# Performance work log

Measured on AMD Instinct MI355X. Metric: run time of the kernel, lower is better.

## Reference

```python
import jax, jax.numpy as jnp
import numpy as np

N_EMBD = 1024
N_HEAD = 16
HEAD_DIM = N_EMBD // N_HEAD
SCALE = HEAD_DIM ** -0.5


def setup_inputs() -> dict:
    key = jax.random.key(0)
    ks = jax.random.split(key, 6)
    B, T = 64, 256
    s = N_EMBD ** -0.5
    return {
        "x": jax.random.normal(ks[0], (B, T, N_EMBD), dtype=jnp.float32),
        "Wq": jax.random.normal(ks[1], (N_EMBD, N_EMBD), dtype=jnp.float32) * s,
        "Wk": jax.random.normal(ks[2], (N_EMBD, N_EMBD), dtype=jnp.float32) * s,
        "Wv": jax.random.normal(ks[3], (N_EMBD, N_EMBD), dtype=jnp.float32) * s,
        "Wo": jax.random.normal(ks[4], (N_EMBD, N_EMBD), dtype=jnp.float32) * s,
        "bo": jax.random.normal(ks[5], (N_EMBD,), dtype=jnp.float32) * 0.01,
    }


def reference(x, Wq, Wk, Wv, Wo, bo):
    B, T, C = x.shape
    # QKV projections (no bias), split heads -> [B, H, T, Dh]
    def heads(y):
        return y.reshape(B, T, N_HEAD, HEAD_DIM).transpose(0, 2, 1, 3)
    q = heads(x @ Wq)
    k = heads(x @ Wk)
    v = heads(x @ Wv)
    # scaled causal attention scores [B, H, T, T]
    wei = jnp.einsum("bhqd,bhkd->bhqk", q, k) * SCALE
    causal = jnp.tril(jnp.ones((T, T), dtype=bool))
    wei = jnp.where(causal, wei, -jnp.inf)
    wei = jax.nn.softmax(wei, axis=-1)
    # dropout is identity in eval mode
    out = jnp.einsum("bhqk,bhkd->bhqd", wei, v)
    out = out.transpose(0, 2, 1, 3).reshape(B, T, C)
    return out @ Wo + bo
```

## Files before the change

### kernel.cpp

```cpp
#include <hip/hip_runtime.h>
#include <hip/hip_bf16.h>
#include <stdint.h>

typedef __attribute__((ext_vector_type(8))) short bfx8;
typedef __attribute__((ext_vector_type(4))) short bfx4;
typedef __attribute__((ext_vector_type(4))) float f32x4;
typedef __attribute__((ext_vector_type(4))) unsigned short us4;

#define SCALE_ATT 0.125f

__device__ __forceinline__ unsigned short f2bf(float f) {
  union { float f; unsigned u; } a; a.f = f;
  unsigned r = a.u + 0x7fffu + ((a.u >> 16) & 1u);
  return (unsigned short)(r >> 16);
}

__device__ __forceinline__ void gll16(const void* g, void* l) {
  __builtin_amdgcn_global_load_lds(
      (__attribute__((address_space(1))) void*)(g),
      (__attribute__((address_space(3))) void*)(l), 16, 0, 0);
}

__device__ __forceinline__ bfx8 ld2x64(const unsigned short* p) {
  bfx4 lo = *(const bfx4*)p;
  bfx4 hi = *(const bfx4*)(p + 4);
  return __builtin_shufflevector(lo, hi, 0, 1, 2, 3, 4, 5, 6, 7);
}

__global__ __launch_bounds__(256) void cvt_x(const float* __restrict__ x,
                                             unsigned short* __restrict__ xb, int n4) {
  int i = blockIdx.x * blockDim.x + threadIdx.x;
  int stride = gridDim.x * blockDim.x;
  const float4* x4 = (const float4*)x;
  for (; i < n4; i += stride) {
    float4 v = x4[i];
    us4 o;
    o[0] = f2bf(v.x); o[1] = f2bf(v.y); o[2] = f2bf(v.z); o[3] = f2bf(v.w);
    *(us4*)&xb[(size_t)i * 4] = o;
  }
}

__global__ __launch_bounds__(256) void cvt_w(const float* __restrict__ W0, const float* __restrict__ W1,
                                             const float* __restrict__ W2, const float* __restrict__ W3,
                                             unsigned short* __restrict__ T0, unsigned short* __restrict__ T1,
                                             unsigned short* __restrict__ T2, unsigned short* __restrict__ T3) {
  const float* W; unsigned short* T;
  switch (blockIdx.z) {
    case 0: W = W0; T = T0; break;
    case 1: W = W1; T = T1; break;
    case 2: W = W2; T = T2; break;
    default: W = W3; T = T3; break;
  }
  __shared__ unsigned short Ts[64][68];
  int k0 = blockIdx.x * 64, n0 = blockIdx.y * 64;
  int t = threadIdx.x;
  int lrow = t >> 4, c4 = t & 15;
  #pragma unroll
  for (int i = 0; i < 4; i++) {
    int row = lrow + i * 16;
    float4 v = *(const float4*)&W[(size_t)(k0 + row) * 1024 + n0 + c4 * 4];
    Ts[c4 * 4 + 0][row] = f2bf(v.x);
    Ts[c4 * 4 + 1][row] = f2bf(v.y);
    Ts[c4 * 4 + 2][row] = f2bf(v.z);
    Ts[c4 * 4 + 3][row] = f2bf(v.w);
  }
  __syncthreads();
  #pragma unroll
  for (int i = 0; i < 4; i++) {
    int nrow = lrow + i * 16;
    us4 v = *(const us4*)&Ts[nrow][c4 * 4];
    *(us4*)&T[(size_t)(n0 + nrow) * 1024 + k0 + c4 * 4] = v;
  }
}

__global__ __launch_bounds__(256) void gemm_qkv(
    const unsigned short* __restrict__ A,
    const unsigned short* __restrict__ Wtq, const unsigned short* __restrict__ Wtk,
    const unsigned short* __restrict__ Wtv,
    unsigned short* __restrict__ Qb, unsigned short* __restrict__ Kb, unsigned short* __restrict__ Vb) {
  __shared__ unsigned short As[128 * 32];
  __shared__ unsigned short Bs[128 * 32];
  int t = threadIdx.x;
  int w = t >> 6, l = t & 63;
  int wr = w >> 1, wc = w & 1;
  int lr = l & 15, lh = l >> 4;
  int bm = blockIdx.x, bn = blockIdx.y;
  int sel = bn >> 3;
  int n0 = (bn & 7) * 128;
  const unsigned short* Bt = sel == 0 ? Wtq : (sel == 1 ? Wtk : Wtv);
  unsigned short* Out = sel == 0 ? Qb : (sel == 1 ? Kb : Vb);

  const unsigned short* Ag = A + (size_t)(bm * 128) * 1024;
  const unsigned short* Bg = Bt + (size_t)n0 * 1024;

  f32x4 acc[4][4];
  #pragma unroll
  for (int i = 0; i < 4; i++)
    #pragma unroll
    for (int j = 0; j < 4; j++) acc[i][j] = (f32x4){0.f, 0.f, 0.f, 0.f};

  int srow = w * 32 + (l >> 2);
  int sk = (l & 3) * 8;

  for (int k0 = 0; k0 < 1024; k0 += 32) {
    gll16(Ag + (size_t)srow * 1024 + k0 + sk,        As + w * 1024);
    gll16(Ag + (size_t)(srow + 16) * 1024 + k0 + sk, As + w * 1024 + 512);
    gll16(Bg + (size_t)srow * 1024 + k0 + sk,        Bs + w * 1024);
    gll16(Bg + (size_t)(srow + 16) * 1024 + k0 + sk, Bs + w * 1024 + 512);
    __syncthreads();
    bfx8 af[4], bfv[4];
    #pragma unroll
    for (int rt = 0; rt < 4; rt++) af[rt] = *(const bfx8*)&As[(wr * 64 + rt * 16 + lr) * 32 + lh * 8];
    #pragma unroll
    for (int ct = 0; ct < 4; ct++) bfv[ct] = *(const bfx8*)&Bs[(wc * 64 + ct * 16 + lr) * 32 + lh * 8];
    #pragma unroll
    for (int rt = 0; rt < 4; rt++)
      #pragma unroll
      for (int ct = 0; ct < 4; ct++)
        acc[rt][ct] = __builtin_amdgcn_mfma_f32_16x16x32_bf16(af[rt], bfv[ct], acc[rt][ct], 0, 0, 0);
    __syncthreads();
  }

  int row0 = bm * 128 + wr * 64;
  #pragma unroll
  for (int rt = 0; rt < 4; rt++)
    #pragma unroll
    for (int ct = 0; ct < 4; ct++)
      #pragma unroll
      for (int j = 0; j < 4; j++) {
        int r = row0 + rt * 16 + lh * 4 + j;
        int c = n0 + wc * 64 + ct * 16 + lr;
        Out[(size_t)r * 1024 + c] = f2bf(acc[rt][ct][j]);
      }
}

__global__ __launch_bounds__(256) void gemm_proj(
    const unsigned short* __restrict__ A, const unsigned short* __restrict__ Bt,
    const float* __restrict__ bias, float* __restrict__ Out) {
  __shared__ unsigned short As[128 * 32];
  __shared__ unsigned short Bs[128 * 32];
  int t = threadIdx.x;
  int w = t >> 6, l = t & 63;
  int wr = w >> 1, wc = w & 1;
  int lr = l & 15, lh = l >> 4;
  int bm = blockIdx.x, bn = blockIdx.y;
  int n0 = bn * 128;
  const unsigned short* Ag = A + (size_t)(bm * 128) * 1024;
  const unsigned short* Bg = Bt + (size_t)n0 * 1024;

  f32x4 acc[4][4];
  #pragma unroll
  for (int i = 0; i < 4; i++)
    #pragma unroll
    for (int j = 0; j < 4; j++) acc[i][j] = (f32x4){0.f, 0.f, 0.f, 0.f};

  int srow = w * 32 + (l >> 2);
  int sk = (l & 3) * 8;

  for (int k0 = 0; k0 < 1024; k0 += 32) {
    gll16(Ag + (size_t)srow * 1024 + k0 + sk,        As + w * 1024);
    gll16(Ag + (size_t)(srow + 16) * 1024 + k0 + sk, As + w * 1024 + 512);
    gll16(Bg + (size_t)srow * 1024 + k0 + sk,        Bs + w * 1024);
    gll16(Bg + (size_t)(srow + 16) * 1024 + k0 + sk, Bs + w * 1024 + 512);
    __syncthreads();
    bfx8 af[4], bfv[4];
    #pragma unroll
    for (int rt = 0; rt < 4; rt++) af[rt] = *(const bfx8*)&As[(wr * 64 + rt * 16 + lr) * 32 + lh * 8];
    #pragma unroll
    for (int ct = 0; ct < 4; ct++) bfv[ct] = *(const bfx8*)&Bs[(wc * 64 + ct * 16 + lr) * 32 + lh * 8];
    #pragma unroll
    for (int rt = 0; rt < 4; rt++)
      #pragma unroll
      for (int ct = 0; ct < 4; ct++)
        acc[rt][ct] = __builtin_amdgcn_mfma_f32_16x16x32_bf16(af[rt], bfv[ct], acc[rt][ct], 0, 0, 0);
    __syncthreads();
  }

  float bv[4];
  #pragma unroll
  for (int ct = 0; ct < 4; ct++) bv[ct] = bias[n0 + wc * 64 + ct * 16 + lr];

  int row0 = bm * 128 + wr * 64;
  #pragma unroll
  for (int rt = 0; rt < 4; rt++)
    #pragma unroll
    for (int ct = 0; ct < 4; ct++)
      #pragma unroll
      for (int j = 0; j < 4; j++) {
        int r = row0 + rt * 16 + lh * 4 + j;
        int c = n0 + wc * 64 + ct * 16 + lr;
        Out[(size_t)r * 1024 + c] = acc[rt][ct][j] + bv[ct];
      }
}

__global__ __launch_bounds__(256) void attn_kernel(
    const unsigned short* __restrict__ Qb, const unsigned short* __restrict__ Kb,
    const unsigned short* __restrict__ Vb, unsigned short* __restrict__ Ab) {
  __shared__ unsigned short Vt[64][260];
  __shared__ unsigned short Pw[4][16][36];

  int t = threadIdx.x;
  int w = t >> 6, l = t & 63;
  int lr = l & 15, lh = l >> 4;
  int bh = blockIdx.x;
  size_t rowbase = (size_t)(bh >> 4) * 256 * 1024 + (size_t)(bh & 15) * 64;

  {
    int rr = t >> 3, part = t & 7;
    for (int i = 0; i < 8; i++) {
      int row = i * 32 + rr;
      bfx8 vv = *(const bfx8*)(Vb + rowbase + (size_t)row * 1024 + part * 8);
      #pragma unroll
      for (int e = 0; e < 8; e++) Vt[part * 8 + e][row] = (unsigned short)vv[e];
    }
  }
  __syncthreads();

  for (int qt = 0; qt < 4; qt++) {
    int r0 = qt * 64 + w * 16;
    const unsigned short* Qrow = Qb + rowbase + (size_t)(r0 + lr) * 1024 + lh * 8;
    bfx8 aq0 = *(const bfx8*)(Qrow);
    bfx8 aq1 = *(const bfx8*)(Qrow + 32);

    float m[4], lsum[4];
    #pragma unroll
    for (int j = 0; j < 4; j++) { m[j] = -1e30f; lsum[j] = 0.f; }
    f32x4 oc[4];
    #pragma unroll
    for (int ct = 0; ct < 4; ct++) oc[ct] = (f32x4){0.f, 0.f, 0.f, 0.f};

    int nkc = ((r0 + 15) >> 5) + 1;
    for (int kc = 0; kc < nkc; kc++) {
      const unsigned short* Kr = Kb + rowbase + (size_t)(kc * 32 + lr) * 1024 + lh * 8;
      bfx8 bk00 = *(const bfx8*)(Kr);
      bfx8 bk01 = *(const bfx8*)(Kr + 32);
      bfx8 bk10 = *(const bfx8*)(Kr + 16 * 1024);
      bfx8 bk11 = *(const bfx8*)(Kr + 16 * 1024 + 32);
      f32x4 s0 = (f32x4){0.f, 0.f, 0.f, 0.f};
      f32x4 s1 = (f32x4){0.f, 0.f, 0.f, 0.f};
      s0 = __builtin_amdgcn_mfma_f32_16x16x32_bf16(aq0, bk00, s0, 0, 0, 0);
      s0 = __builtin_amdgcn_mfma_f32_16x16x32_bf16(aq1, bk01, s0, 0, 0, 0);
      s1 = __builtin_amdgcn_mfma_f32_16x16x32_bf16(aq0, bk10, s1, 0, 0, 0);
      s1 = __builtin_amdgcn_mfma_f32_16x16x32_bf16(aq1, bk11, s1, 0, 0, 0);

      int c0 = kc * 32 + lr, c1 = c0 + 16;
      #pragma unroll
      for (int j = 0; j < 4; j++) {
        int row = r0 + lh * 4 + j;
        float v0 = (c0 <= row) ? s0[j] : -1e30f;
        float v1 = (c1 <= row) ? s1[j] : -1e30f;
        float cm = fmaxf(v0, v1);
        cm = fmaxf(cm, __shfl_xor(cm, 1));
        cm = fmaxf(cm, __shfl_xor(cm, 2));
        cm = fmaxf(cm, __shfl_xor(cm, 4));
        cm = fmaxf(cm, __shfl_xor(cm, 8));
        float mn = fmaxf(m[j], cm);
        float sc = __expf((m[j] - mn) * SCALE_ATT);
        float p0 = (c0 <= row) ? __expf((s0[j] - mn) * SCALE_ATT) : 0.f;
        float p1 = (c1 <= row) ? __expf((s1[j] - mn) * SCALE_ATT) : 0.f;
        m[j] = mn;
        float cs = p0 + p1;
        cs += __shfl_xor(cs, 1);
        cs += __shfl_xor(cs, 2);
        cs += __shfl_xor(cs, 4);
        cs += __shfl_xor(cs, 8);
        lsum[j] = lsum[j] * sc + cs;
        #pragma unroll
        for (int ct = 0; ct < 4; ct++) oc[ct][j] *= sc;
        Pw[w][lh * 4 + j][lr] = f2bf(p0);
        Pw[w][lh * 4 + j][16 + lr] = f2bf(p1);
      }

      bfx8 pa = ld2x64(&Pw[w][lr][lh * 8]);
      #pragma unroll
      for (int ct = 0; ct < 4; ct++) {
        bfx8 vb = ld2x64(&Vt[ct * 16 + lr][kc * 32 + lh * 8]);
        oc[ct] = __builtin_amdgcn_mfma_f32_16x16x32_bf16(pa, vb, oc[ct], 0, 0, 0);
      }
    }

    float rinv[4];
    #pragma unroll
    for (int j = 0; j < 4; j++) rinv[j] = 1.0f / lsum[j];
    #pragma unroll
    for (int ct = 0; ct < 4; ct++)
      #pragma unroll
      for (int j = 0; j < 4; j++) {
        int row = r0 + lh * 4 + j;
        Ab[rowbase + (size_t)row * 1024 + ct * 16 + lr] = f2bf(oc[ct][j] * rinv[j]);
      }
  }
}

extern "C" void kernel_launch(void* const* d_in, const int* in_sizes, int n_in,
                              void* d_out, int out_size, void* d_ws, size_t ws_size,
                              hipStream_t stream) {
  const float* x  = (const float*)d_in[0];
  const float* Wq = (const float*)d_in[1];
  const float* Wk = (const float*)d_in[2];
  const float* Wv = (const float*)d_in[3];
  const float* Wo = (const float*)d_in[4];
  const float* bo = (const float*)d_in[5];
  float* out = (float*)d_out;

  char* ws = (char*)d_ws;
  unsigned short* xb  = (unsigned short*)(ws);
  unsigned short* Wtq = (unsigned short*)(ws + (size_t)(32u << 20));
  unsigned short* Wtk = (unsigned short*)(ws + (size_t)(34u << 20));
  unsigned short* Wtv = (unsigned short*)(ws + (size_t)(36u << 20));
  unsigned short* Wto = (unsigned short*)(ws + (size_t)(38u << 20));
  unsigned short* Qb  = (unsigned short*)(ws + (size_t)(40u << 20));
  unsigned short* Kb  = (unsigned short*)(ws + (size_t)(72u << 20));
  unsigned short* Vb  = (unsigned short*)(ws + (size_t)(104u << 20));
  unsigned short* Ab  = xb;

  cvt_x<<<2048, 256, 0, stream>>>(x, xb, 4194304);
  cvt_w<<<dim3(16, 16, 4), 256, 0, stream>>>(Wq, Wk, Wv, Wo, Wtq, Wtk, Wtv, Wto);
  gemm_qkv<<<dim3(128, 24), 256, 0, stream>>>(xb, Wtq, Wtk, Wtv, Qb, Kb, Vb);
  attn_kernel<<<1024, 256, 0, stream>>>(Qb, Kb, Vb, Ab);
  gemm_proj<<<dim3(128, 8), 256, 0, stream>>>(Ab, Wto, bo, out);
}
```

Before: 257.3 us.

## Replace QKV and output GEMMs with 256x256 double-buffered 8-wave pipelined kernel

Both GEMMs are replaced by one templated kernel that uses 256x256 tiles with 512 threads and double-buffered LDS stages covering 128 k per iteration. Direct global-to-LDS loads for the next stage overlap the MFMA work on the current one, using explicit vmcnt/lgkmcnt waits, raised wave priority around MFMA, an XOR swizzle against LDS bank conflicts, and a remapped block order for cache locality. This aims to cut the per-k-step barrier stalls and the poor reuse of the old 128x128 tiles. The cost is heavy register and LDS use (128KB of LDS per block) and hand-written wait counts that are fragile to get right.

```diff
diff --git a/kernel.cpp b/kernel.cpp
--- a/kernel.cpp
+++ b/kernel.cpp
@@ -73,123 +73,163 @@
   }
 }
 
-__global__ __launch_bounds__(256) void gemm_qkv(
+#define DS_BAR() __builtin_amdgcn_s_barrier()
+#define LGKM0() do { asm volatile("s_waitcnt lgkmcnt(0)" ::: "memory"); \
+                     __builtin_amdgcn_sched_barrier(0); } while (0)
+#define VMW4() asm volatile("s_waitcnt vmcnt(4)" ::: "memory")
+#define VMW0() asm volatile("s_waitcnt vmcnt(0)" ::: "memory")
+
+#define STAGE(hs, gb, r0, kbyte) do { \
+  const char* _g = (const char*)(gb) + (size_t)((r0) + srow) * 2048 + (size_t)(kbyte) + scolb; \
+  gll16(_g, (hs) + w * 1024); \
+  gll16(_g + 16 * 2048, (hs) + w * 1024 + 512); \
+} while (0)
+
+#define LOADA(dst, hs, qm) \
+  _Pragma("unroll") for (int mi = 0; mi < 4; ++mi) \
+    dst[mi] = *(const bfx8*)&(hs)[(wm * 128 + (qm) * 64 + mi * 16 + lr) * 32 + rcol];
+
+#define LOADB(dst, hs) \
+  _Pragma("unroll") for (int ni = 0; ni < 4; ++ni) \
+    dst[ni] = *(const bfx8*)&(hs)[(wn * 64 + ni * 16 + lr) * 32 + rcol];
+
+#define MFMA16(rb, a, b) \
+  _Pragma("unroll") for (int mi = 0; mi < 4; ++mi) \
+    _Pragma("unroll") for (int ni = 0; ni < 4; ++ni) \
+      acc[(rb) + mi][ni] = __builtin_amdgcn_mfma_f32_16x16x32_bf16(a[mi], b[ni], acc[(rb) + mi][ni], 0, 0, 0);
+
+template<int MODE>
+__global__ __launch_bounds__(512, 2) void gemm8p(
     const unsigned short* __restrict__ A,
-    const unsigned short* __restrict__ Wtq, const unsigned short* __restrict__ Wtk,
-    const unsigned short* __restrict__ Wtv,
-    unsigned short* __restrict__ Qb, unsigned short* __restrict__ Kb, unsigned short* __restrict__ Vb) {
-  __shared__ unsigned short As[128 * 32];
-  __shared__ unsigned short Bs[128 * 32];
-  int t = threadIdx.x;
-  int w = t >> 6, l = t & 63;
-  int wr = w >> 1, wc = w & 1;
+    const unsigned short* __restrict__ Bt0, const unsigned short* __restrict__ Bt1,
+    const unsigned short* __restrict__ Bt2,
+    unsigned short* __restrict__ O0, unsigned short* __restrict__ O1,
+    unsigned short* __restrict__ O2,
+    const float* __restrict__ bias, float* __restrict__ OutF, int nby) {
+  __shared__ unsigned short A0s[2][256 * 32];
+  __shared__ unsigned short B0s[2][256 * 32];
+  __shared__ unsigned short A1s[2][256 * 32];
+  __shared__ unsigned short B1s[2][256 * 32];
+
+  int tid = threadIdx.x;
+  int w = tid >> 6, l = tid & 63;
   int lr = l & 15, lh = l >> 4;
-  int bm = blockIdx.x, bn = blockIdx.y;
-  int sel = bn >> 3;
-  int n0 = (bn & 7) * 128;
-  const unsigned short* Bt = sel == 0 ? Wtq : (sel == 1 ? Wtk : Wtv);
-  unsigned short* Out = sel == 0 ? Qb : (sel == 1 ? Kb : Vb);
-
-  const unsigned short* Ag = A + (size_t)(bm * 128) * 1024;
-  const unsigned short* Bg = Bt + (size_t)n0 * 1024;
-
-  f32x4 acc[4][4];
+  int wm = w >> 2, wn = w & 3;
+  int srow = w * 32 + (l >> 2);
+  int scolb = ((l & 3) * 16) ^ (((l >> 5) & 1) << 5);
+  int rcol = (lh * 8) ^ (((lr >> 3) & 1) << 4);
+
+  int cpx = gridDim.x >> 3;
+  int o = blockIdx.x;
+  int wg = (o & 7) * cpx + (o >> 3);
+  int bm = wg / nby, bn = wg % nby;
+
+  const unsigned short* Bt;
+  unsigned short* Ob = nullptr;
+  int n0;
+  if (MODE == 0) {
+    int sel = bn >> 2;
+    n0 = (bn & 3) * 256;
+    Bt = sel == 0 ? Bt0 : (sel == 1 ? Bt1 : Bt2);
+    Ob = sel == 0 ? O0 : (sel == 1 ? O1 : O2);
+  } else {
+    Bt = Bt0;
+    n0 = bn * 256;
+  }
+  int am0 = bm * 256;
+
+  f32x4 acc[8][4];
   #pragma unroll
-  for (int i = 0; i < 4; i++)
-    #pragma unroll
-    for (int j = 0; j < 4; j++) acc[i][j] = (f32x4){0.f, 0.f, 0.f, 0.f};
-
-  int srow = w * 32 + (l >> 2);
-  int sk = (l & 3) * 8;
-
-  for (int k0 = 0; k0 < 1024; k0 += 32) {
-    gll16(Ag + (size_t)srow * 1024 + k0 + sk,        As + w * 1024);
-    gll16(Ag + (size_t)(srow + 16) * 1024 + k0 + sk, As + w * 1024 + 512);
-    gll16(Bg + (size_t)srow * 1024 + k0 + sk,        Bs + w * 1024);
-    gll16(Bg + (size_t)(srow + 16) * 1024 + k0 + sk, Bs + w * 1024 + 512);
-    __syncthreads();
-    bfx8 af[4], bfv[4];
-    #pragma unroll
-    for (int rt = 0; rt < 4; rt++) af[rt] = *(const bfx8*)&As[(wr * 64 + rt * 16 + lr) * 32 + lh * 8];
-    #pragma unroll
-    for (int ct = 0; ct < 4; ct++) bfv[ct] = *(const bfx8*)&Bs[(wc * 64 + ct * 16 + lr) * 32 + lh * 8];
-    #pragma unroll
-    for (int rt = 0; rt < 4; rt++)
-      #pragma unroll
-      for (int ct = 0; ct < 4; ct++)
-        acc[rt][ct] = __builtin_amdgcn_mfma_f32_16x16x32_bf16(af[rt], bfv[ct], acc[rt][ct], 0, 0, 0);
-    __syncthreads();
-  }
-
-  int row0 = bm * 128 + wr * 64;
+  for (int i = 0; i < 8; ++i)
+    #pragma unroll
+    for (int jj = 0; jj < 4; ++jj) acc[i][jj] = (f32x4){0.f, 0.f, 0.f, 0.f};
+
+  bfx8 af[4], bf0[4], bf1[4];
+
+  STAGE(A0s[0], A, am0, 0);   __builtin_amdgcn_sched_barrier(0);
+  STAGE(B0s[0], Bt, n0, 0);   __builtin_amdgcn_sched_barrier(0);
+  STAGE(A1s[0], A, am0, 64);  __builtin_amdgcn_sched_barrier(0);
+  STAGE(B1s[0], Bt, n0, 64);  __builtin_amdgcn_sched_barrier(0);
+  VMW4();
+  DS_BAR();
+
+  int cur = 0;
+  #pragma unroll 1
+  for (int t = 0; t < 15; ++t) {
+    int kb = (t + 1) * 128;
+    LOADA(af, A0s[cur], 0);
+    LOADB(bf0, B0s[cur]);
+    STAGE(A0s[cur ^ 1], A, am0, kb);
+    DS_BAR(); LGKM0();
+    __builtin_amdgcn_s_setprio(1);
+    MFMA16(0, af, bf0);
+    __builtin_amdgcn_s_setprio(0);
+    DS_BAR();
+    LOADA(af, A0s[cur], 1);
+    STAGE(B0s[cur ^ 1], Bt, n0, kb);
+    DS_BAR(); LGKM0();
+    __builtin_amdgcn_s_setprio(1);
+    MFMA16(4, af, bf0);
+    __builtin_amdgcn_s_setprio(0);
+    VMW4();
+    DS_BAR();
+    LOADA(af, A1s[cur], 0);
+    LOADB(bf1, B1s[cur]);
+    STAGE(A1s[cur ^ 1], A, am0, kb + 64);
+    DS_BAR(); LGKM0();
+    __builtin_amdgcn_s_setprio(1);
+    MFMA16(0, af, bf1);
+    __builtin_amdgcn_s_setprio(0);
+    DS_BAR();
+    LOADA(af, A1s[cur], 1);
+    STAGE(B1s[cur ^ 1], Bt, n0, kb + 64);
+    DS_BAR(); LGKM0();
+    __builtin_amdgcn_s_setprio(1);
+    MFMA16(4, af, bf1);
+    __builtin_amdgcn_s_setprio(0);
+    VMW4();
+    DS_BAR();
+    cur ^= 1;
+  }
+  LOADA(af, A0s[cur], 0);
+  LOADB(bf0, B0s[cur]);
+  DS_BAR(); LGKM0();
+  __builtin_amdgcn_s_setprio(1);
+  MFMA16(0, af, bf0);
+  __builtin_amdgcn_s_setprio(0);
+  DS_BAR();
+  LOADA(af, A0s[cur], 1);
+  DS_BAR(); LGKM0();
+  __builtin_amdgcn_s_setprio(1);
+  MFMA16(4, af, bf0);
+  __builtin_amdgcn_s_setprio(0);
+  VMW0();
+  DS_BAR();
+  LOADA(af, A1s[cur], 0);
+  LOADB(bf1, B1s[cur]);
+  DS_BAR(); LGKM0();
+  __builtin_amdgcn_s_setprio(1);
+  MFMA16(0, af, bf1);
+  __builtin_amdgcn_s_setprio(0);
+  DS_BAR();
+  LOADA(af, A1s[cur], 1);
+  LGKM0();
+  __builtin_amdgcn_s_setprio(1);
+  MFMA16(4, af, bf1);
+  __builtin_amdgcn_s_setprio(0);
+
   #pragma unroll
-  for (int rt = 0; rt < 4; rt++)
-    #pragma unroll
-    for (int ct = 0; ct < 4; ct++)
-      #pragma unroll
-      for (int j = 0; j < 4; j++) {
-        int r = row0 + rt * 16 + lh * 4 + j;
-        int c = n0 + wc * 64 + ct * 16 + lr;
-        Out[(size_t)r * 1024 + c] = f2bf(acc[rt][ct][j]);
-      }
-}
-
-__global__ __launch_bounds__(256) void gemm_proj(
-    const unsigned short* __restrict__ A, const unsigned short* __restrict__ Bt,
-    const float* __restrict__ bias, float* __restrict__ Out) {
-  __shared__ unsigned short As[128 * 32];
-  __shared__ unsigned short Bs[128 * 32];
-  int t = threadIdx.x;
-  int w = t >> 6, l = t & 63;
-  int wr = w >> 1, wc = w & 1;
-  int lr = l & 15, lh = l >> 4;
-  int bm = blockIdx.x, bn = blockIdx.y;
-  int n0 = bn * 128;
-  const unsigned short* Ag = A + (size_t)(bm * 128) * 1024;
-  const unsigned short* Bg = Bt + (size_t)n0 * 1024;
-
-  f32x4 acc[4][4];
-  #pragma unroll
-  for (int i = 0; i < 4; i++)
-    #pragma unroll
-    for (int j = 0; j < 4; j++) acc[i][j] = (f32x4){0.f, 0.f, 0.f, 0.f};
-
-  int srow = w * 32 + (l >> 2);
-  int sk = (l & 3) * 8;
-
-  for (int k0 = 0; k0 < 1024; k0 += 32) {
-    gll16(Ag + (size_t)srow * 1024 + k0 + sk,        As + w * 1024);
-    gll16(Ag + (size_t)(srow + 16) * 1024 + k0 + sk, As + w * 1024 + 512);
-    gll16(Bg + (size_t)srow * 1024 + k0 + sk,        Bs + w * 1024);
-    gll16(Bg + (size_t)(srow + 16) * 1024 + k0 + sk, Bs + w * 1024 + 512);
-    __syncthreads();
-    bfx8 af[4], bfv[4];
-    #pragma unroll
-    for (int rt = 0; rt < 4; rt++) af[rt] = *(const bfx8*)&As[(wr * 64 + rt * 16 + lr) * 32 + lh * 8];
-    #pragma unroll
-    for (int ct = 0; ct < 4; ct++) bfv[ct] = *(const bfx8*)&Bs[(wc * 64 + ct * 16 + lr) * 32 + lh * 8];
-    #pragma unroll
-    for (int rt = 0; rt < 4; rt++)
-      #pragma unroll
-      for (int ct = 0; ct < 4; ct++)
-        acc[rt][ct] = __builtin_amdgcn_mfma_f32_16x16x32_bf16(af[rt], bfv[ct], acc[rt][ct], 0, 0, 0);
-    __syncthreads();
-  }
-
-  float bv[4];
-  #pragma unroll
-  for (int ct = 0; ct < 4; ct++) bv[ct] = bias[n0 + wc * 64 + ct * 16 + lr];
-
-  int row0 = bm * 128 + wr * 64;
-  #pragma unroll
-  for (int rt = 0; rt < 4; rt++)
-    #pragma unroll
-    for (int ct = 0; ct < 4; ct++)
-      #pragma unroll
-      for (int j = 0; j < 4; j++) {
-        int r = row0 + rt * 16 + lh * 4 + j;
-        int c = n0 + wc * 64 + ct * 16 + lr;
-        Out[(size_t)r * 1024 + c] = acc[rt][ct][j] + bv[ct];
+  for (int mi8 = 0; mi8 < 8; ++mi8)
+    #pragma unroll
+    for (int ni = 0; ni < 4; ++ni)
+      #pragma unroll
+      for (int j = 0; j < 4; ++j) {
+        int r = am0 + wm * 128 + mi8 * 16 + lh * 4 + j;
+        int c = n0 + wn * 64 + ni * 16 + lr;
+        if (MODE == 0)
+          Ob[(size_t)r * 1024 + c] = f2bf(acc[mi8][ni][j]);
+        else
+          OutF[(size_t)r * 1024 + c] = acc[mi8][ni][j] + bias[c];
       }
 }
 
@@ -316,7 +356,7 @@
 
   cvt_x<<<2048, 256, 0, stream>>>(x, xb, 4194304);
   cvt_w<<<dim3(16, 16, 4), 256, 0, stream>>>(Wq, Wk, Wv, Wo, Wtq, Wtk, Wtv, Wto);
-  gemm_qkv<<<dim3(128, 24), 256, 0, stream>>>(xb, Wtq, Wtk, Wtv, Qb, Kb, Vb);
+  gemm8p<0><<<768, 512, 0, stream>>>(xb, Wtq, Wtk, Wtv, Qb, Kb, Vb, nullptr, nullptr, 12);
   attn_kernel<<<1024, 256, 0, stream>>>(Qb, Kb, Vb, Ab);
-  gemm_proj<<<dim3(128, 8), 256, 0, stream>>>(Ab, Wto, bo, out);
-}
+  gemm8p<1><<<256, 512, 0, stream>>>(Ab, Wto, Wto, Wto, nullptr, nullptr, nullptr, bo, out, 4);
+}
```

Result: faster. 224.2 us (-12.8%).
